# Performance work log

Hardware: AMD Instinct MI355X
Metric: run time of the kernel (lower is better)

## Reference

```python
import jax, jax.numpy as jnp
import numpy as np

B, G, N, C = 4, 64, 256, 256
HEAD = 8
HD = C // HEAD  # 32


def setup_inputs() -> dict:
    key = jax.random.key(0)
    ks = jax.random.split(key, 11)
    s = 0.02
    return {
        "q": jax.random.normal(ks[0], (B, G, N, C), jnp.float32),
        "k": jax.random.normal(ks[1], (B, G, N, C), jnp.float32),
        "v": jax.random.normal(ks[2], (B, G, N, C), jnp.float32),
        "wq": jax.random.normal(ks[3], (C, C), jnp.float32) * s,
        "bq": jnp.zeros((C,), jnp.float32),
        "wk": jax.random.normal(ks[4], (C, C), jnp.float32) * s,
        "bk": jnp.zeros((C,), jnp.float32),
        "wv": jax.random.normal(ks[5], (C, C), jnp.float32) * s,
        "bv": jnp.zeros((C,), jnp.float32),
        "wo": jax.random.normal(ks[6], (C, C), jnp.float32) * s,
        "bo": jnp.zeros((C,), jnp.float32),
    }


def reference(q, k, v, wq, bq, wk, bk, wv, bv, wo, bo):
    # Linear projections (torch Linear == x @ W.T + b; here W stored as (in,out))
    Q = q @ wq + bq  # (B,G,N,C)
    K = k @ wk + bk
    V = v @ wv + bv
    # split heads: (B,G,N,C) -> (B,G,N,H,hd)
    Qh = Q.reshape(B, G, N, HEAD, HD)
    Kh = K.reshape(B, G, N, HEAD, HD)
    Vh = V.reshape(B, G, N, HEAD, HD)
    scale = jnp.sqrt(jnp.float32(HD)) + 1e-8
    # scores: per batch b, head h, group g: (N,N)
    score = jnp.einsum("bgnhd,bgmhd->bhgnm", Qh, Kh) / scale
    attn = jax.nn.softmax(score, axis=-1)
    ctx = jnp.einsum("bhgnm,bgmhd->bgnhd", attn, Vh)  # (B,G,N,H,hd)
    ctx = ctx.reshape(B, G, N, C)
    # output projection (dropout = identity in eval)
    return ctx @ wo + bo
```

## Files before the change

kernel.cpp:

```cpp
#include <hip/hip_runtime.h>
#include <hip/hip_bf16.h>
#include <cstdint>
#include <cstddef>


typedef __attribute__((ext_vector_type(4))) float f4;
typedef __attribute__((ext_vector_type(8))) short s8;
typedef __attribute__((ext_vector_type(4))) short s4;
typedef unsigned short u16;

#define AS1 __attribute__((address_space(1)))
#define AS3 __attribute__((address_space(3)))

static constexpr int CD = 256;

__device__ __forceinline__ u16 f2bf(float f) {
    __hip_bfloat16 h = __float2bfloat16(f);
    return *reinterpret_cast<u16*>(&h);
}

__device__ __forceinline__ void gload_lds16(const void* g, void* l) {
    __builtin_amdgcn_global_load_lds((const AS1 uint32_t*)g, (AS3 uint32_t*)l, 16, 0, 0);
}

__global__ __launch_bounds__(256) void prep_k(const float* __restrict__ wq,
                                              const float* __restrict__ wk,
                                              const float* __restrict__ wv,
                                              const float* __restrict__ wo,
                                              u16* __restrict__ WT, float qs)
{
    const int bx = blockIdx.x;
    const int wsel = bx >> 4, tl = bx & 15;
    const int k0 = (tl & 3) * 64, n0 = (tl >> 2) * 64;
    const float* W = wsel == 0 ? wq : wsel == 1 ? wk : wsel == 2 ? wv : wo;
    const float scale = wsel == 0 ? qs : 1.0f;
    u16* dst = WT + (size_t)wsel * 65536;
    __shared__ float T[64][65];
    const int t = threadIdx.x;
    const int rr = t >> 4, c0 = (t & 15) * 4;
    #pragma unroll
    for (int i = 0; i < 4; ++i) {
        int r = i * 16 + rr;
        f4 f = *(const f4*)(W + (size_t)(k0 + r) * CD + n0 + c0);
        #pragma unroll
        for (int j = 0; j < 4; ++j) T[c0 + j][r] = f[j] * scale;
    }
    __syncthreads();
    #pragma unroll
    for (int i = 0; i < 4; ++i) {
        int n = i * 16 + rr;
        s4 h;
        #pragma unroll
        for (int j = 0; j < 4; ++j) h[j] = (short)f2bf(T[n][c0 + j]);
        *(s4*)(dst + (size_t)(n0 + n) * CD + k0 + c0) = h;
    }
}

template<bool A_F32, bool OUT_F32>
__device__ __forceinline__ void gemm_body(const void* __restrict__ Ain,
                                          const u16* __restrict__ Wt,
                                          const float* __restrict__ bias,
                                          float escale, void* __restrict__ Out,
                                          int d)
{
    __shared__ u16 As[2][128 * 64];
    __shared__ u16 Bs[2][128 * 64];
    const int t = threadIdx.x, lane = t & 63, w = t >> 6;
    const int n0 = (d >> 9) * 128;
    const int m0 = (d & 511) * 128;
    const int wr = (w >> 1) * 64, wc = (w & 1) * 64;
    const int lr = lane & 15, lk = (lane >> 4) * 8;
    const int bc = lane >> 3, bcol = (lane & 7) * 8;

    f4 acc[4][4] = {};
    f4 pa[8];

    auto stageB = [&](int k0, int buf) {
        #pragma unroll
        for (int j = 0; j < 4; ++j) {
            int c = j * 4 + w;
            int row = c * 8 + bc;
            int col = bcol ^ ((row & 7) << 3);
            gload_lds16(Wt + (size_t)(n0 + row) * CD + k0 + col,
                        &Bs[buf][c * 512 + lane * 8]);
        }
    };
    auto stageA16 = [&](int k0, int buf) {
        const u16* A = (const u16*)Ain;
        #pragma unroll
        for (int j = 0; j < 4; ++j) {
            int c = j * 4 + w;
            int row = c * 8 + bc;
            int col = bcol ^ ((row & 7) << 3);
            gload_lds16(A + (size_t)(m0 + row) * CD + k0 + col,
                        &As[buf][c * 512 + lane * 8]);
        }
    };
    auto loadA = [&](int k0) {
        const float* A = (const float*)Ain;
        #pragma unroll
        for (int j = 0; j < 4; ++j) {
            int ch = t + j * 256;
            int r = ch >> 3, c8 = ch & 7;
            const float* src = A + (size_t)(m0 + r) * CD + k0 + c8 * 8;
            pa[2 * j]     = *(const f4*)src;
            pa[2 * j + 1] = *(const f4*)(src + 4);
        }
    };
    auto writeA = [&](int buf) {
        #pragma unroll
        for (int j = 0; j < 4; ++j) {
            int ch = t + j * 256;
            int r = ch >> 3, c8 = ch & 7;
            s8 h;
            #pragma unroll
            for (int i = 0; i < 4; ++i) {
                h[i]     = (short)f2bf(pa[2 * j][i]);
                h[i + 4] = (short)f2bf(pa[2 * j + 1][i]);
            }
            *(s8*)&As[buf][r * 64 + ((c8 * 8) ^ ((r & 7) << 3))] = h;
        }
    };
    auto compute = [&](int buf) {
        #pragma unroll
        for (int kk = 0; kk < 64; kk += 32) {
            s8 a[4], b[4];
            #pragma unroll
            for (int m = 0; m < 4; ++m) {
                int R = wr + m * 16 + lr;
                a[m] = *(const s8*)&As[buf][R * 64 + ((kk + lk) ^ ((R & 7) << 3))];
            }
            #pragma unroll
            for (int n = 0; n < 4; ++n) {
                int R = wc + n * 16 + lr;
                b[n] = *(const s8*)&Bs[buf][R * 64 + ((kk + lk) ^ ((R & 7) << 3))];
            }
            #pragma unroll
            for (int m = 0; m < 4; ++m)
                #pragma unroll
                for (int n = 0; n < 4; ++n)
                    acc[m][n] = __builtin_amdgcn_mfma_f32_16x16x32_bf16(
                        a[m], b[n], acc[m][n], 0, 0, 0);
        }
    };

    stageB(0, 0);
    if constexpr (A_F32) { loadA(0); writeA(0); } else { stageA16(0, 0); }
    __syncthreads();

    #pragma unroll
    for (int ti = 0; ti < 4; ++ti) {
        const int cur = ti & 1, nxt = cur ^ 1;
        const int kn = (ti + 1) * 64;
        if (ti < 3) {
            if constexpr (A_F32) loadA(kn); else stageA16(kn, nxt);
            stageB(kn, nxt);
        }
        compute(cur);
        if (ti < 3) {
            if constexpr (A_F32) writeA(nxt);
        }
        __syncthreads();
    }

    const int orow = (lane >> 4) * 4;
    #pragma unroll
    for (int n = 0; n < 4; ++n) {
        int col = n0 + wc + n * 16 + lr;
        float bb = bias[col] * escale;
        #pragma unroll
        for (int m = 0; m < 4; ++m)
            #pragma unroll
            for (int r = 0; r < 4; ++r) {
                int row = m0 + wr + m * 16 + orow + r;
                float vv = acc[m][n][r] + bb;
                if constexpr (OUT_F32)
                    ((float*)Out)[(size_t)row * CD + col] = vv;
                else
                    ((u16*)Out)[(size_t)row * CD + col] = f2bf(vv);
            }
    }
}

__global__ __launch_bounds__(256, 2) void gemmqkv_k(const float* q, const float* k,
        const float* v, const u16* WT, const float* bq, const float* bk,
        const float* bv, float qs, u16* Qb, u16* Kb, u16* Vb)
{
    const int op = blockIdx.x >> 10;
    const int d  = blockIdx.x & 1023;
    const float* A    = op == 0 ? q  : op == 1 ? k  : v;
    const u16*   Wt   = WT + (size_t)op * 65536;
    const float* bias = op == 0 ? bq : op == 1 ? bk : bv;
    u16*         Out  = op == 0 ? Qb : op == 1 ? Kb : Vb;
    gemm_body<true, false>(A, Wt, bias, op == 0 ? qs : 1.0f, Out, d);
}

__global__ __launch_bounds__(256, 2) void gemmo_k(const u16* Cx, const u16* WT,
                                                  const float* bo, float* out)
{
    gemm_body<false, true>(Cx, WT, bo, 1.0f, out, blockIdx.x);
}

__global__ __launch_bounds__(256, 3) void attn_k(const u16* Qb,
                                                 const u16* __restrict__ Kb,
                                                 const u16* __restrict__ Vb,
                                                 u16* Ctx)
{
    __shared__ u16 Ks[256 * 32];
    __shared__ u16 Vt[32][260];
    __shared__ u16 Ps[4][16][132];
    const int d = blockIdx.x;
    const int bg = d & 255, h = d >> 8;
    const size_t base = (size_t)bg * (256 * 256) + h * 32;
    const int t = threadIdx.x, lane = t & 63, w = t >> 6;
    const int lr = lane & 15, lk = (lane >> 4) * 8;
    const int orow = (lane >> 4) * 4;

    #pragma unroll
    for (int j = 0; j < 4; ++j) {
        int c = j * 4 + w;
        int row = c * 16 + (lane >> 2);
        int col = ((lane & 3) * 8) ^ (((row >> 1) & 3) << 3);
        gload_lds16(Kb + base + (size_t)row * CD + col, &Ks[c * 512 + lane * 8]);
    }
    {
        int n0 = (t >> 2) * 4, c0 = (t & 3) * 8;
        const u16* vp = Vb + base + (size_t)n0 * CD + c0;
        s8 r0 = *(const s8*)(vp);
        s8 r1 = *(const s8*)(vp + CD);
        s8 r2 = *(const s8*)(vp + 2 * CD);
        s8 r3 = *(const s8*)(vp + 3 * CD);
        #pragma unroll
        for (int i = 0; i < 8; ++i) {
            s4 cv = { r0[i], r1[i], r2[i], r3[i] };
            *(s4*)&Vt[c0 + i][n0] = cv;
        }
    }
    s8 aq[4];
    #pragma unroll
    for (int m = 0; m < 4; ++m)
        aq[m] = *(const s8*)(Qb + base + (size_t)(w * 64 + m * 16 + lr) * CD + lk);

    __syncthreads();

    const int myslot = lk ^ (((lr >> 1) & 3) << 3);
    const f4 zero = {0.f, 0.f, 0.f, 0.f};

    #pragma unroll
    for (int m = 0; m < 4; ++m) {
        f4 s[16];
        #pragma unroll
        for (int j = 0; j < 16; ++j) {
            s8 bk = *(const s8*)&Ks[(j * 16 + lr) * 32 + myslot];
            s[j] = __builtin_amdgcn_mfma_f32_16x16x32_bf16(aq[m], bk, zero, 0, 0, 0);
        }
        float mrow[4] = {-3.0e38f, -3.0e38f, -3.0e38f, -3.0e38f};
        #pragma unroll
        for (int j = 0; j < 16; ++j)
            #pragma unroll
            for (int r = 0; r < 4; ++r) mrow[r] = fmaxf(mrow[r], s[j][r]);
        #pragma unroll
        for (int dd = 1; dd < 16; dd <<= 1)
            #pragma unroll
            for (int r = 0; r < 4; ++r) mrow[r] = fmaxf(mrow[r], __shfl_xor(mrow[r], dd));
        float lsum[4] = {0.f, 0.f, 0.f, 0.f};
        #pragma unroll
        for (int j = 0; j < 16; ++j)
            #pragma unroll
            for (int r = 0; r < 4; ++r) {
                float p = exp2f(s[j][r] - mrow[r]);
                s[j][r] = p;
                lsum[r] += p;
            }
        #pragma unroll
        for (int dd = 1; dd < 16; dd <<= 1)
            #pragma unroll
            for (int r = 0; r < 4; ++r) lsum[r] += __shfl_xor(lsum[r], dd);

        f4 o0 = zero, o1 = zero;
        #pragma unroll
        for (int half = 0; half < 2; ++half) {
            #pragma unroll
            for (int j = 0; j < 8; ++j)
                #pragma unroll
                for (int r = 0; r < 4; ++r)
                    Ps[w][orow + r][j * 16 + lr] = f2bf(s[half * 8 + j][r]);
            #pragma unroll
            for (int kk = 0; kk < 4; ++kk) {
                s8 ap  = *(const s8*)&Ps[w][lr][kk * 32 + lk];
                s8 bv0 = *(const s8*)&Vt[lr][(half * 4 + kk) * 32 + lk];
                s8 bv1 = *(const s8*)&Vt[16 + lr][(half * 4 + kk) * 32 + lk];
                o0 = __builtin_amdgcn_mfma_f32_16x16x32_bf16(ap, bv0, o0, 0, 0, 0);
                o1 = __builtin_amdgcn_mfma_f32_16x16x32_bf16(ap, bv1, o1, 0, 0, 0);
            }
        }
        #pragma unroll
        for (int r = 0; r < 4; ++r) {
            float inv = __builtin_amdgcn_rcpf(lsum[r]);
            int row = w * 64 + m * 16 + orow + r;
            Ctx[base + (size_t)row * CD + lr]      = f2bf(o0[r] * inv);
            Ctx[base + (size_t)row * CD + 16 + lr] = f2bf(o1[r] * inv);
        }
    }
}

extern "C" void kernel_launch(void* const* d_in, const int* in_sizes, int n_in,
                              void* d_out, int out_size, void* d_ws, size_t ws_size,
                              hipStream_t stream) {
    const float* q  = (const float*)d_in[0];
    const float* k  = (const float*)d_in[1];
    const float* v  = (const float*)d_in[2];
    const float* wq = (const float*)d_in[3];
    const float* bq = (const float*)d_in[4];
    const float* wk = (const float*)d_in[5];
    const float* bk = (const float*)d_in[6];
    const float* wv = (const float*)d_in[7];
    const float* bv = (const float*)d_in[8];
    const float* wo = (const float*)d_in[9];
    const float* bo = (const float*)d_in[10];
    float* out = (float*)d_out;

    const size_t E = (size_t)65536 * 256;
    u16* Qb = (u16*)d_ws;
    u16* Kb = Qb + E;
    u16* Vb = Kb + E;
    u16* WT = Vb + E;
    u16* Cx = Qb;

    const float qs = (1.0f / (sqrtf(32.0f) + 1e-8f)) * 1.4426950408889634f;

    prep_k<<<64, 256, 0, stream>>>(wq, wk, wv, wo, WT, qs);
    gemmqkv_k<<<3072, 256, 0, stream>>>(q, k, v, WT, bq, bk, bv, qs, Qb, Kb, Vb);
    attn_k<<<2048, 256, 0, stream>>>(Qb, Kb, Vb, Cx);
    gemmo_k<<<1024, 256, 0, stream>>>(Cx, WT + 3 * 65536, bo, out);
}
```

Measured before the change: 193.8 us.

## Single-buffer GEMM LDS, raise occupancy, transpose MFMA for vectorized stores

Replaces the double-buffered LDS tiles in the shared GEMM body with single buffers, halving LDS use per block, and raises launch bounds from 2 to 4 blocks per SIMD for the QKV and output projection kernels. The loop now computes, syncs, then stages the next tile and syncs again, so within a block there is no load/compute overlap and the design depends on more resident blocks to hide latency. The MFMA operands are swapped so each lane holds four consecutive columns, which lets the epilogue use vector bias loads and 4-wide stores instead of scalar strided stores. The higher occupancy target may force register pressure or spills with 64 accumulator floats per thread.

```diff
diff --git a/kernel.cpp b/kernel.cpp
--- a/kernel.cpp
+++ b/kernel.cpp
@@ -63,29 +63,30 @@
                                           float escale, void* __restrict__ Out,
                                           int d)
 {
-    __shared__ u16 As[2][128 * 64];
-    __shared__ u16 Bs[2][128 * 64];
+    __shared__ u16 As[128 * 64];
+    __shared__ u16 Bs[128 * 64];
     const int t = threadIdx.x, lane = t & 63, w = t >> 6;
     const int n0 = (d >> 9) * 128;
     const int m0 = (d & 511) * 128;
     const int wr = (w >> 1) * 64, wc = (w & 1) * 64;
-    const int lr = lane & 15, lk = (lane >> 4) * 8;
+    const int lr = lane & 15, lkg = lane >> 4;
+    const int lk = lkg * 8;
     const int bc = lane >> 3, bcol = (lane & 7) * 8;
 
     f4 acc[4][4] = {};
     f4 pa[8];
 
-    auto stageB = [&](int k0, int buf) {
+    auto stageB = [&](int k0) {
         #pragma unroll
         for (int j = 0; j < 4; ++j) {
             int c = j * 4 + w;
             int row = c * 8 + bc;
             int col = bcol ^ ((row & 7) << 3);
             gload_lds16(Wt + (size_t)(n0 + row) * CD + k0 + col,
-                        &Bs[buf][c * 512 + lane * 8]);
-        }
-    };
-    auto stageA16 = [&](int k0, int buf) {
+                        &Bs[c * 512 + lane * 8]);
+        }
+    };
+    auto stageA16 = [&](int k0) {
         const u16* A = (const u16*)Ain;
         #pragma unroll
         for (int j = 0; j < 4; ++j) {
@@ -93,7 +94,7 @@
             int row = c * 8 + bc;
             int col = bcol ^ ((row & 7) << 3);
             gload_lds16(A + (size_t)(m0 + row) * CD + k0 + col,
-                        &As[buf][c * 512 + lane * 8]);
+                        &As[c * 512 + lane * 8]);
         }
     };
     auto loadA = [&](int k0) {
@@ -107,7 +108,7 @@
             pa[2 * j + 1] = *(const f4*)(src + 4);
         }
     };
-    auto writeA = [&](int buf) {
+    auto writeA = [&]() {
         #pragma unroll
         for (int j = 0; j < 4; ++j) {
             int ch = t + j * 256;
@@ -118,71 +119,71 @@
                 h[i]     = (short)f2bf(pa[2 * j][i]);
                 h[i + 4] = (short)f2bf(pa[2 * j + 1][i]);
             }
-            *(s8*)&As[buf][r * 64 + ((c8 * 8) ^ ((r & 7) << 3))] = h;
-        }
-    };
-    auto compute = [&](int buf) {
+            *(s8*)&As[r * 64 + ((c8 * 8) ^ ((r & 7) << 3))] = h;
+        }
+    };
+    auto compute = [&]() {
         #pragma unroll
         for (int kk = 0; kk < 64; kk += 32) {
             s8 a[4], b[4];
             #pragma unroll
             for (int m = 0; m < 4; ++m) {
                 int R = wr + m * 16 + lr;
-                a[m] = *(const s8*)&As[buf][R * 64 + ((kk + lk) ^ ((R & 7) << 3))];
+                a[m] = *(const s8*)&As[R * 64 + ((kk + lk) ^ ((R & 7) << 3))];
             }
             #pragma unroll
             for (int n = 0; n < 4; ++n) {
                 int R = wc + n * 16 + lr;
-                b[n] = *(const s8*)&Bs[buf][R * 64 + ((kk + lk) ^ ((R & 7) << 3))];
+                b[n] = *(const s8*)&Bs[R * 64 + ((kk + lk) ^ ((R & 7) << 3))];
             }
             #pragma unroll
             for (int m = 0; m < 4; ++m)
                 #pragma unroll
                 for (int n = 0; n < 4; ++n)
                     acc[m][n] = __builtin_amdgcn_mfma_f32_16x16x32_bf16(
-                        a[m], b[n], acc[m][n], 0, 0, 0);
-        }
-    };
-
-    stageB(0, 0);
-    if constexpr (A_F32) { loadA(0); writeA(0); } else { stageA16(0, 0); }
+                        b[n], a[m], acc[m][n], 0, 0, 0);
+        }
+    };
+
+    if constexpr (A_F32) { loadA(0); stageB(0); writeA(); }
+    else { stageA16(0); stageB(0); }
     __syncthreads();
 
     #pragma unroll
     for (int ti = 0; ti < 4; ++ti) {
-        const int cur = ti & 1, nxt = cur ^ 1;
-        const int kn = (ti + 1) * 64;
+        if constexpr (A_F32) { if (ti < 3) loadA((ti + 1) * 64); }
+        compute();
+        __syncthreads();
         if (ti < 3) {
-            if constexpr (A_F32) loadA(kn); else stageA16(kn, nxt);
-            stageB(kn, nxt);
-        }
-        compute(cur);
-        if (ti < 3) {
-            if constexpr (A_F32) writeA(nxt);
-        }
-        __syncthreads();
-    }
-
-    const int orow = (lane >> 4) * 4;
-    #pragma unroll
-    for (int n = 0; n < 4; ++n) {
-        int col = n0 + wc + n * 16 + lr;
-        float bb = bias[col] * escale;
-        #pragma unroll
-        for (int m = 0; m < 4; ++m)
-            #pragma unroll
-            for (int r = 0; r < 4; ++r) {
-                int row = m0 + wr + m * 16 + orow + r;
-                float vv = acc[m][n][r] + bb;
-                if constexpr (OUT_F32)
-                    ((float*)Out)[(size_t)row * CD + col] = vv;
-                else
-                    ((u16*)Out)[(size_t)row * CD + col] = f2bf(vv);
-            }
-    }
-}
-
-__global__ __launch_bounds__(256, 2) void gemmqkv_k(const float* q, const float* k,
+            if constexpr (A_F32) { writeA(); stageB((ti + 1) * 64); }
+            else { stageA16((ti + 1) * 64); stageB((ti + 1) * 64); }
+            __syncthreads();
+        }
+    }
+
+    #pragma unroll
+    for (int m = 0; m < 4; ++m) {
+        int row = m0 + wr + m * 16 + lr;
+        #pragma unroll
+        for (int n = 0; n < 4; ++n) {
+            int col0 = n0 + wc + n * 16 + lkg * 4;
+            f4 bb = *(const f4*)&bias[col0];
+            f4 vv;
+            #pragma unroll
+            for (int r = 0; r < 4; ++r) vv[r] = acc[m][n][r] + bb[r] * escale;
+            if constexpr (OUT_F32) {
+                *(f4*)&((float*)Out)[(size_t)row * CD + col0] = vv;
+            } else {
+                s4 h;
+                #pragma unroll
+                for (int r = 0; r < 4; ++r) h[r] = (short)f2bf(vv[r]);
+                *(s4*)&((u16*)Out)[(size_t)row * CD + col0] = h;
+            }
+        }
+    }
+}
+
+__global__ __launch_bounds__(256, 4) void gemmqkv_k(const float* q, const float* k,
         const float* v, const u16* WT, const float* bq, const float* bk,
         const float* bv, float qs, u16* Qb, u16* Kb, u16* Vb)
 {
@@ -195,7 +196,7 @@
     gemm_body<true, false>(A, Wt, bias, op == 0 ? qs : 1.0f, Out, d);
 }
 
-__global__ __launch_bounds__(256, 2) void gemmo_k(const u16* Cx, const u16* WT,
+__global__ __launch_bounds__(256, 4) void gemmo_k(const u16* Cx, const u16* WT,
                                                   const float* bo, float* out)
 {
     gemm_body<false, true>(Cx, WT, bo, 1.0f, out, blockIdx.x);
```

Result: faster. 183.8 us (-5.1%).
